# Kernel tuning notes

Hardware: AMD Instinct MI355X
Metric: run time of the kernel (lower is better)

## Reference

```python
import jax, jax.numpy as jnp
import numpy as np

B, L, D = 4096, 50, 64
NU, NI, NR = 100000, 100000, 5


def setup_inputs() -> dict:
    key = jax.random.key(0)
    ks = jax.random.split(key, 16)
    s = 0.02
    inp = {
        "nodes_v": jax.random.randint(ks[0], (B,), 0, NI),
        "neigh_u": jax.random.randint(ks[1], (B, L), 0, NU),
        "neigh_r": jax.random.randint(ks[2], (B, L), 0, NR),
        "embed_u": jax.random.normal(ks[3], (NU, D)) * s,
        "embed_i": jax.random.normal(ks[4], (NI, D)) * s,
        "embed_r": jax.random.normal(ks[5], (NR, D)) * s,
        # gv MLP: Linear(2D,D) ReLU Linear(D,D) ReLU Linear(D,D)
        "gv_w1": jax.random.normal(ks[6], (2 * D, D)) * s, "gv_b1": jnp.zeros((D,)),
        "gv_w2": jax.random.normal(ks[7], (D, D)) * s,     "gv_b2": jnp.zeros((D,)),
        "gv_w3": jax.random.normal(ks[8], (D, D)) * s,     "gv_b3": jnp.zeros((D,)),
        # attention MLP: Linear(2D,D) ReLU Linear(D,D) ReLU Linear(D,1), softmax over neighbors
        "att_w1": jax.random.normal(ks[9], (2 * D, D)) * s, "att_b1": jnp.zeros((D,)),
        "att_w2": jax.random.normal(ks[10], (D, D)) * s,    "att_b2": jnp.zeros((D,)),
        "att_w3": jax.random.normal(ks[11], (D, 1)) * s,    "att_b3": jnp.zeros((1,)),
        # combine: Linear(2D,D) ReLU Linear(D,D) ReLU
        "wr1_w": jax.random.normal(ks[12], (2 * D, D)) * s, "wr1_b": jnp.zeros((D,)),
        "wr2_w": jax.random.normal(ks[13], (D, D)) * s,     "wr2_b": jnp.zeros((D,)),
    }
    return inp


def reference(nodes_v, neigh_u, neigh_r, embed_u, embed_i, embed_r,
              gv_w1, gv_b1, gv_w2, gv_b2, gv_w3, gv_b3,
              att_w1, att_b1, att_w2, att_b2, att_w3, att_b3,
              wr1_w, wr1_b, wr2_w, wr2_b):
    qj = embed_i[nodes_v]            # [B, D] item reps
    pt = embed_u[neigh_u]            # [B, L, D] neighbor user reps
    er = embed_r[neigh_r]            # [B, L, D] rating reps
    # fusion MLP g(.)
    x = jnp.concatenate([pt, er], axis=-1)                    # [B, L, 2D]
    h = jax.nn.relu(x @ gv_w1 + gv_b1)
    h = jax.nn.relu(h @ gv_w2 + gv_b2)
    fjt = h @ gv_w3 + gv_b3                                   # [B, L, D]
    # attention over neighbors (dropout is identity in eval mode)
    q_rep = jnp.broadcast_to(qj[:, None, :], fjt.shape)       # [B, L, D]
    a = jnp.concatenate([fjt, q_rep], axis=-1)                # [B, L, 2D]
    a = jax.nn.relu(a @ att_w1 + att_b1)
    a = jax.nn.relu(a @ att_w2 + att_b2)
    scores = (a @ att_w3 + att_b3)[..., 0]                    # [B, L]
    mu = jax.nn.softmax(scores, axis=1)                       # softmax over neighbors
    zj = jnp.einsum("bld,bl->bd", fjt, mu)                   # weighted aggregation
    # combine aggregated neighborhood with item's own embedding (2D -> D)
    z = jax.nn.relu(jnp.concatenate([zj, qj], axis=-1) @ wr1_w + wr1_b)
    out = jax.nn.relu(z @ wr2_w + wr2_b)                      # [B, D]
    return out
```

## Files before the change

kernel.cpp:

```cpp
#include <hip/hip_runtime.h>

typedef __bf16 bf16;
typedef short s16x8 __attribute__((ext_vector_type(8)));
typedef __bf16 b16x8 __attribute__((ext_vector_type(8)));
typedef float f32x4 __attribute__((ext_vector_type(4)));

#define B_   4096
#define L_   50
#define SH   72

#define OFF_W1F  0
#define OFF_W2F  8192
#define OFF_W3F  12288
#define OFF_WCF  16384
#define OFF_A2F  20480
#define OFF_R1T  24576
#define OFF_R2T  32768
#define WT_TOTAL 36864
#define BIAS1P_BYTE 73728
#define CQ_BYTE     73984
#define EU16_BYTE   1122560
#define ER16_BYTE   13922560
#define WS_NEED     13923200

#define PREP_W_BLOCKS 145
#define CQ_BLOCKS     32
#define CONV_THREADS  800040
#define CONV_BLOCKS   3126

__device__ __forceinline__ unsigned short f2b(float f) {
    __bf16 h = (__bf16)f;
    return __builtin_bit_cast(unsigned short, h);
}
__device__ __forceinline__ unsigned pack2(float a, float b) {
    return (unsigned)f2b(a) | ((unsigned)f2b(b) << 16);
}
__device__ __forceinline__ s16x8 mkfrag(float4 a, float4 b) {
    union { s16x8 v; unsigned u[4]; } r;
    r.u[0] = pack2(a.x, a.y); r.u[1] = pack2(a.z, a.w);
    r.u[2] = pack2(b.x, b.y); r.u[3] = pack2(b.z, b.w);
    return r.v;
}
__device__ __forceinline__ f32x4 mfma16(s16x8 a, s16x8 b, f32x4 c) {
    return __builtin_amdgcn_mfma_f32_16x16x32_bf16(a, b, c, 0, 0, 0);
}

extern "C" __global__ void prep_all(const float* __restrict__ w1, const float* __restrict__ w2,
                                    const float* __restrict__ w3, const float* __restrict__ a1,
                                    const float* __restrict__ a2, const float* __restrict__ r1,
                                    const float* __restrict__ r2, const float* __restrict__ gb3,
                                    const float* __restrict__ ab1,
                                    const int* __restrict__ nodes_v, const float* __restrict__ embed_i,
                                    const float* __restrict__ embed_u, const float* __restrict__ embed_r,
                                    bf16* __restrict__ wt, float* __restrict__ bias1p,
                                    float* __restrict__ cq,
                                    bf16* __restrict__ eu16, bf16* __restrict__ er16)
{
    if (blockIdx.x >= PREP_W_BLOCKS + CQ_BLOCKS) {
        long t = (long)(blockIdx.x - PREP_W_BLOCKS - CQ_BLOCKS) * 256 + threadIdx.x;
        if (t < 800000) {
            const float* s = embed_u + t * 8;
            float4 a = *(const float4*)s, b = *(const float4*)(s + 4);
            *(s16x8*)(eu16 + t * 8) = mkfrag(a, b);
        } else if (t < CONV_THREADS) {
            long r = (t - 800000) * 8;
            const float* s = embed_r + r;
            float4 a = *(const float4*)s, b = *(const float4*)(s + 4);
            *(s16x8*)(er16 + r) = mkfrag(a, b);
        }
        return;
    }
    if (blockIdx.x >= PREP_W_BLOCKS) {
        int wv   = (blockIdx.x - PREP_W_BLOCKS) * 4 + (threadIdx.x >> 6);
        int lane = threadIdx.x & 63, m = lane & 15, quad = lane >> 4;
        int base = wv * 32;
        int i0 = base + m, i1 = base + 16 + m;
        int v0 = nodes_v[i0], v1 = nodes_v[i1];

        s16x8 bfr[8];
#pragma unroll
        for (int kt = 0; kt < 2; ++kt)
#pragma unroll
            for (int nt = 0; nt < 4; ++nt) {
                const float* src = a1 + (64 + kt * 32 + quad * 8) * 64 + nt * 16 + m;
                union { s16x8 v; unsigned u[4]; } fr;
#pragma unroll
                for (int jj = 0; jj < 4; ++jj)
                    fr.u[jj] = pack2(src[(2 * jj) * 64], src[(2 * jj + 1) * 64]);
                bfr[kt * 4 + nt] = fr.v;
            }

        f32x4 ac0[4] = {}, ac1[4] = {};
#pragma unroll
        for (int kt = 0; kt < 2; ++kt) {
            const float* q0 = embed_i + (size_t)v0 * 64 + kt * 32 + quad * 8;
            const float* q1 = embed_i + (size_t)v1 * 64 + kt * 32 + quad * 8;
            s16x8 aq0 = mkfrag(*(const float4*)q0, *(const float4*)(q0 + 4));
            s16x8 aq1 = mkfrag(*(const float4*)q1, *(const float4*)(q1 + 4));
#pragma unroll
            for (int nt = 0; nt < 4; ++nt) {
                ac0[nt] = mfma16(aq0, bfr[kt * 4 + nt], ac0[nt]);
                ac1[nt] = mfma16(aq1, bfr[kt * 4 + nt], ac1[nt]);
            }
        }
#pragma unroll
        for (int nt = 0; nt < 4; ++nt) {
            int c = nt * 16 + m;
#pragma unroll
            for (int r4 = 0; r4 < 4; ++r4) {
                cq[(base + quad * 4 + r4) * 64 + c]      = ac0[nt][r4];
                cq[(base + 16 + quad * 4 + r4) * 64 + c] = ac1[nt][r4];
            }
        }
        return;
    }
    int i = blockIdx.x * 256 + threadIdx.x;
    if (i >= WT_TOTAL + 64) return;
    if (i >= WT_TOTAL) {
        int n = i - WT_TOTAL;
        float s0 = ab1[n], s1 = 0.f, s2 = 0.f, s3 = 0.f;
#pragma unroll
        for (int t = 0; t < 64; t += 4) {
            s0 = fmaf(gb3[t],     a1[t * 64 + n],       s0);
            s1 = fmaf(gb3[t + 1], a1[(t + 1) * 64 + n], s1);
            s2 = fmaf(gb3[t + 2], a1[(t + 2) * 64 + n], s2);
            s3 = fmaf(gb3[t + 3], a1[(t + 3) * 64 + n], s3);
        }
        bias1p[n] = (s0 + s1) + (s2 + s3);
        return;
    }
    float val;
    if (i < OFF_R1T) {
        int off, kind;
        if      (i < OFF_W2F) { off = OFF_W1F; kind = 0; }
        else if (i < OFF_W3F) { off = OFF_W2F; kind = 1; }
        else if (i < OFF_WCF) { off = OFF_W3F; kind = 2; }
        else if (i < OFF_A2F) { off = OFF_WCF; kind = 3; }
        else                  { off = OFF_A2F; kind = 4; }
        int local = i - off;
        int f = local >> 9, lane = (local >> 3) & 63, j = local & 7;
        int kt = f >> 2, nt = f & 3, quad = lane >> 4, m = lane & 15;
        int k = kt * 32 + quad * 8 + j;
        int n = nt * 16 + m;
        if (kind == 0)      val = w1[k * 64 + n];
        else if (kind == 1) val = w2[k * 64 + n];
        else if (kind == 2) val = w3[k * 64 + n];
        else if (kind == 4) val = a2[k * 64 + n];
        else {
            float s0 = 0.f, s1 = 0.f, s2 = 0.f, s3 = 0.f;
#pragma unroll
            for (int t = 0; t < 64; t += 4) {
                float4 w = *(const float4*)(w3 + k * 64 + t);
                s0 = fmaf(w.x, a1[t * 64 + n],       s0);
                s1 = fmaf(w.y, a1[(t + 1) * 64 + n], s1);
                s2 = fmaf(w.z, a1[(t + 2) * 64 + n], s2);
                s3 = fmaf(w.w, a1[(t + 3) * 64 + n], s3);
            }
            val = (s0 + s1) + (s2 + s3);
        }
    }
    else if (i < OFF_R2T) { int li = i - OFF_R1T; int n = li >> 7, k = li & 127; val = r1[k * 64 + n]; }
    else                  { int li = i - OFF_R2T; int n = li >> 6, k = li & 63;  val = r2[k * 64 + n]; }
    wt[i] = (bf16)val;
}

template<bool BF16E>
__global__ void __launch_bounds__(256, 2)
dense_fused(const int* __restrict__ nodes_v, const int* __restrict__ neigh_u,
            const int* __restrict__ neigh_r,
            const float* __restrict__ embed_u, const float* __restrict__ embed_i,
            const float* __restrict__ embed_r,
            const float* __restrict__ gv_b1, const float* __restrict__ gv_b2,
            const float* __restrict__ gv_b3,
            const float* __restrict__ att_b2, const float* __restrict__ att_w3,
            const float* __restrict__ wr1_b, const float* __restrict__ wr2_b,
            const bf16* __restrict__ wt, const bf16* __restrict__ eu16,
            const bf16* __restrict__ er16, const float* __restrict__ cq,
            const float* __restrict__ bias1p, float* __restrict__ out)
{
    __shared__ __align__(16) bf16 H[128 * SH];
    __shared__ float zp[4 * 64];
    __shared__ float swm[4 * 2];
    __shared__ float qsh[2 * 64];

    const int tid = threadIdx.x;
    const int lane = tid & 63, wave = tid >> 6;
    const int m = lane & 15, quad = lane >> 4;
    const int b0 = blockIdx.x * 2;
    const int rw0 = wave * 32;
    const int item_w = rw0 >> 6;
    const int lbase = rw0 & 63;

    const int bw = b0 + item_w;
    const int l0 = min(lbase + m, L_ - 1);
    const int l1 = min(lbase + 16 + m, L_ - 1);
    const int u0 = neigh_u[bw * L_ + l0], u1 = neigh_u[bw * L_ + l1];
    const int v0 = neigh_r[bw * L_ + l0], v1 = neigh_r[bw * L_ + l1];

    float cs4[4];
#pragma unroll
    for (int nt = 0; nt < 4; ++nt) {
        int c = nt * 16 + m;
        cs4[nt] = cq[bw * 64 + c] + bias1p[c];
    }

    bf16* Hw = H + rw0 * SH;
    bf16* H0 = Hw;
    bf16* H1 = Hw + 16 * SH;

    {
        f32x4 ac0[4] = {}, ac1[4] = {};
        if constexpr (BF16E) {
            const bf16* p00 = eu16 + (size_t)u0 * 64;
            const bf16* p01 = eu16 + (size_t)u1 * 64;
            const bf16* p10 = er16 + v0 * 64;
            const bf16* p11 = er16 + v1 * 64;
#pragma unroll
            for (int kt = 0; kt < 4; ++kt) {
                const bf16* s0p = (kt < 2 ? p00 : p10) + (kt & 1) * 32 + quad * 8;
                const bf16* s1p = (kt < 2 ? p01 : p11) + (kt & 1) * 32 + quad * 8;
                s16x8 a0 = *(const s16x8*)s0p;
                s16x8 a1 = *(const s16x8*)s1p;
#pragma unroll
                for (int nt = 0; nt < 4; ++nt) {
                    s16x8 bfr = *(const s16x8*)(wt + OFF_W1F + (kt * 4 + nt) * 512 + lane * 8);
                    ac0[nt] = mfma16(a0, bfr, ac0[nt]);
                    ac1[nt] = mfma16(a1, bfr, ac1[nt]);
                }
            }
        } else {
            const float* b00 = embed_u + (size_t)u0 * 64;
            const float* b01 = embed_u + (size_t)u1 * 64;
            const float* b10 = embed_r + v0 * 64;
            const float* b11 = embed_r + v1 * 64;
#pragma unroll
            for (int kt = 0; kt < 4; ++kt) {
                const float* s0p = (kt < 2 ? b00 : b10) + (kt & 1) * 32 + quad * 8;
                const float* s1p = (kt < 2 ? b01 : b11) + (kt & 1) * 32 + quad * 8;
                float4 a0a = *(const float4*)s0p, a0b = *(const float4*)(s0p + 4);
                float4 a1a = *(const float4*)s1p, a1b = *(const float4*)(s1p + 4);
                s16x8 a0 = mkfrag(a0a, a0b);
                s16x8 a1 = mkfrag(a1a, a1b);
#pragma unroll
                for (int nt = 0; nt < 4; ++nt) {
                    s16x8 bfr = *(const s16x8*)(wt + OFF_W1F + (kt * 4 + nt) * 512 + lane * 8);
                    ac0[nt] = mfma16(a0, bfr, ac0[nt]);
                    ac1[nt] = mfma16(a1, bfr, ac1[nt]);
                }
            }
        }
#pragma unroll
        for (int nt = 0; nt < 4; ++nt) {
            int c = nt * 16 + m;
            float bv = gv_b1[c];
#pragma unroll
            for (int r4 = 0; r4 < 4; ++r4) {
                H0[(quad * 4 + r4) * SH + c] = (bf16)fmaxf(ac0[nt][r4] + bv, 0.f);
                H1[(quad * 4 + r4) * SH + c] = (bf16)fmaxf(ac1[nt][r4] + bv, 0.f);
            }
        }
    }

    {
        f32x4 ac0[4] = {}, ac1[4] = {};
#pragma unroll
        for (int kt = 0; kt < 2; ++kt) {
            s16x8 a0 = *(const s16x8*)(H0 + m * SH + kt * 32 + quad * 8);
            s16x8 a1 = *(const s16x8*)(H1 + m * SH + kt * 32 + quad * 8);
#pragma unroll
            for (int nt = 0; nt < 4; ++nt) {
                s16x8 bfr = *(const s16x8*)(wt + OFF_W2F + (kt * 4 + nt) * 512 + lane * 8);
                ac0[nt] = mfma16(a0, bfr, ac0[nt]);
                ac1[nt] = mfma16(a1, bfr, ac1[nt]);
            }
        }
#pragma unroll
        for (int nt = 0; nt < 4; ++nt) {
            int c = nt * 16 + m;
            float bv = gv_b2[c];
#pragma unroll
            for (int r4 = 0; r4 < 4; ++r4) {
                H0[(quad * 4 + r4) * SH + c] = (bf16)fmaxf(ac0[nt][r4] + bv, 0.f);
                H1[(quad * 4 + r4) * SH + c] = (bf16)fmaxf(ac1[nt][r4] + bv, 0.f);
            }
        }
    }

    f32x4 aF0[4] = {}, aF1[4] = {};
    {
        f32x4 aA0[4] = {}, aA1[4] = {};
#pragma unroll
        for (int kt = 0; kt < 2; ++kt) {
            s16x8 a0 = *(const s16x8*)(H0 + m * SH + kt * 32 + quad * 8);
            s16x8 a1 = *(const s16x8*)(H1 + m * SH + kt * 32 + quad * 8);
#pragma unroll
            for (int nt = 0; nt < 4; ++nt) {
                s16x8 bF = *(const s16x8*)(wt + OFF_W3F + (kt * 4 + nt) * 512 + lane * 8);
                s16x8 bA = *(const s16x8*)(wt + OFF_WCF + (kt * 4 + nt) * 512 + lane * 8);
                aF0[nt] = mfma16(a0, bF, aF0[nt]);
                aF1[nt] = mfma16(a1, bF, aF1[nt]);
                aA0[nt] = mfma16(a0, bA, aA0[nt]);
                aA1[nt] = mfma16(a1, bA, aA1[nt]);
            }
        }
#pragma unroll
        for (int nt = 0; nt < 4; ++nt) {
            int c = nt * 16 + m;
#pragma unroll
            for (int r4 = 0; r4 < 4; ++r4) {
                H0[(quad * 4 + r4) * SH + c] = (bf16)fmaxf(aA0[nt][r4] + cs4[nt], 0.f);
                H1[(quad * 4 + r4) * SH + c] = (bf16)fmaxf(aA1[nt][r4] + cs4[nt], 0.f);
            }
        }
    }

    float s0[4], s1[4];
    {
        f32x4 ac0[4] = {}, ac1[4] = {};
#pragma unroll
        for (int kt = 0; kt < 2; ++kt) {
            s16x8 a0 = *(const s16x8*)(H0 + m * SH + kt * 32 + quad * 8);
            s16x8 a1 = *(const s16x8*)(H1 + m * SH + kt * 32 + quad * 8);
#pragma unroll
            for (int nt = 0; nt < 4; ++nt) {
                s16x8 bfr = *(const s16x8*)(wt + OFF_A2F + (kt * 4 + nt) * 512 + lane * 8);
                ac0[nt] = mfma16(a0, bfr, ac0[nt]);
                ac1[nt] = mfma16(a1, bfr, ac1[nt]);
            }
        }
#pragma unroll
        for (int r4 = 0; r4 < 4; ++r4) { s0[r4] = 0.f; s1[r4] = 0.f; }
#pragma unroll
        for (int nt = 0; nt < 4; ++nt) {
            int c = nt * 16 + m;
            float b2v = att_b2[c], w3v = att_w3[c];
#pragma unroll
            for (int r4 = 0; r4 < 4; ++r4) {
                s0[r4] += fmaxf(ac0[nt][r4] + b2v, 0.f) * w3v;
                s1[r4] += fmaxf(ac1[nt][r4] + b2v, 0.f) * w3v;
            }
        }
#pragma unroll
        for (int mask = 1; mask < 16; mask <<= 1)
#pragma unroll
            for (int r4 = 0; r4 < 4; ++r4) {
                s0[r4] += __shfl_xor(s0[r4], mask);
                s1[r4] += __shfl_xor(s1[r4], mask);
            }
    }

    {
        const int r0b = lbase + quad * 4;
        float mloc = -1e30f;
#pragma unroll
        for (int r4 = 0; r4 < 4; ++r4) {
            if (r0b + r4 < L_)      mloc = fmaxf(mloc, s0[r4]);
            if (r0b + 16 + r4 < L_) mloc = fmaxf(mloc, s1[r4]);
        }
        mloc = fmaxf(mloc, __shfl_xor(mloc, 16));
        mloc = fmaxf(mloc, __shfl_xor(mloc, 32));

        float e0[4], e1[4], ssum = 0.f;
#pragma unroll
        for (int r4 = 0; r4 < 4; ++r4) {
            e0[r4] = (r0b + r4 < L_)      ? __expf(s0[r4] - mloc) : 0.f;
            e1[r4] = (r0b + 16 + r4 < L_) ? __expf(s1[r4] - mloc) : 0.f;
            ssum += e0[r4] + e1[r4];
        }
        ssum += __shfl_xor(ssum, 16);
        ssum += __shfl_xor(ssum, 32);

        float z[4] = {0.f, 0.f, 0.f, 0.f};
#pragma unroll
        for (int r4 = 0; r4 < 4; ++r4)
#pragma unroll
            for (int nt = 0; nt < 4; ++nt)
                z[nt] += aF0[nt][r4] * e0[r4] + aF1[nt][r4] * e1[r4];
#pragma unroll
        for (int nt = 0; nt < 4; ++nt) {
            z[nt] += __shfl_xor(z[nt], 16);
            z[nt] += __shfl_xor(z[nt], 32);
        }
        if (quad == 0) {
#pragma unroll
            for (int nt = 0; nt < 4; ++nt) zp[wave * 64 + nt * 16 + m] = z[nt];
        }
        if (lane == 0) { swm[wave * 2] = ssum; swm[wave * 2 + 1] = mloc; }
    }
    __syncthreads();

    if ((wave & 1) == 0) {
        const int item = wave >> 1;
        const int d = lane;
        float ma = swm[wave * 2 + 1],      mb = swm[(wave + 1) * 2 + 1];
        float sa = swm[wave * 2],          sb = swm[(wave + 1) * 2];
        float M  = fmaxf(ma, mb);
        float fa = __expf(ma - M), fb = __expf(mb - M);
        float zj = (fa * zp[wave * 64 + d] + fb * zp[(wave + 1) * 64 + d])
                 / (fa * sa + fb * sb) + gv_b3[d];

        float* zsh = zp + wave * 64;
        zsh[d] = zj;
        qsh[item * 64 + d] = embed_i[nodes_v[b0 + item] * 64 + d];

        float accz = wr1_b[d];
        const bf16* r1 = wt + OFF_R1T + d * 128;
#pragma unroll
        for (int k8 = 0; k8 < 8; ++k8) {
            b16x8 wv = *(const b16x8*)(r1 + k8 * 8);
#pragma unroll
            for (int j = 0; j < 8; ++j) accz = fmaf((float)wv[j], zsh[k8 * 8 + j], accz);
        }
#pragma unroll
        for (int k8 = 0; k8 < 8; ++k8) {
            b16x8 wv = *(const b16x8*)(r1 + 64 + k8 * 8);
#pragma unroll
            for (int j = 0; j < 8; ++j) accz = fmaf((float)wv[j], qsh[item * 64 + k8 * 8 + j], accz);
        }
        zsh[d] = fmaxf(accz, 0.f);

        float acco = wr2_b[d];
        const bf16* r2 = wt + OFF_R2T + d * 64;
#pragma unroll
        for (int k8 = 0; k8 < 8; ++k8) {
            b16x8 wv = *(const b16x8*)(r2 + k8 * 8);
#pragma unroll
            for (int j = 0; j < 8; ++j) acco = fmaf((float)wv[j], zsh[k8 * 8 + j], acco);
        }
        out[(b0 + item) * 64 + d] = fmaxf(acco, 0.f);
    }
}

extern "C" void kernel_launch(void* const* d_in, const int* in_sizes, int n_in,
                              void* d_out, int out_size, void* d_ws, size_t ws_size,
                              hipStream_t stream)
{
    const int* nodes_v = (const int*)d_in[0];
    const int* neigh_u = (const int*)d_in[1];
    const int* neigh_r = (const int*)d_in[2];
    const float* embed_u = (const float*)d_in[3];
    const float* embed_i = (const float*)d_in[4];
    const float* embed_r = (const float*)d_in[5];
    const float* gv_w1  = (const float*)d_in[6];  const float* gv_b1 = (const float*)d_in[7];
    const float* gv_w2  = (const float*)d_in[8];  const float* gv_b2 = (const float*)d_in[9];
    const float* gv_w3  = (const float*)d_in[10]; const float* gv_b3 = (const float*)d_in[11];
    const float* att_w1 = (const float*)d_in[12]; const float* att_b1 = (const float*)d_in[13];
    const float* att_w2 = (const float*)d_in[14]; const float* att_b2 = (const float*)d_in[15];
    const float* att_w3 = (const float*)d_in[16]; const float* att_b3 = (const float*)d_in[17];
    const float* wr1_w  = (const float*)d_in[18]; const float* wr1_b = (const float*)d_in[19];
    const float* wr2_w  = (const float*)d_in[20]; const float* wr2_b = (const float*)d_in[21];
    (void)att_b3;

    bf16*  wt     = (bf16*)d_ws;
    float* bias1p = (float*)((char*)d_ws + BIAS1P_BYTE);
    float* cq     = (float*)((char*)d_ws + CQ_BYTE);
    bf16*  eu16   = (bf16*)((char*)d_ws + EU16_BYTE);
    bf16*  er16   = (bf16*)((char*)d_ws + ER16_BYTE);

    const bool big = ws_size >= (size_t)WS_NEED;
    const int prep_grid = PREP_W_BLOCKS + CQ_BLOCKS + (big ? CONV_BLOCKS : 0);

    prep_all<<<prep_grid, 256, 0, stream>>>(
        gv_w1, gv_w2, gv_w3, att_w1, att_w2, wr1_w, wr2_w, gv_b3, att_b1,
        nodes_v, embed_i, embed_u, embed_r, wt, bias1p, cq, eu16, er16);

    if (big) {
        dense_fused<true><<<B_ / 2, 256, 0, stream>>>(nodes_v, neigh_u, neigh_r,
                                                      embed_u, embed_i, embed_r,
                                                      gv_b1, gv_b2, gv_b3, att_b2, att_w3,
                                                      wr1_b, wr2_b, wt, eu16, er16,
                                                      cq, bias1p, (float*)d_out);
    } else {
        dense_fused<false><<<B_ / 2, 256, 0, stream>>>(nodes_v, neigh_u, neigh_r,
                                                       embed_u, embed_i, embed_r,
                                                       gv_b1, gv_b2, gv_b3, att_b2, att_w3,
                                                       wr1_b, wr2_b, wt, eu16, er16,
                                                       cq, bias1p, (float*)d_out);
    }
}
```

Baseline: 159.3 us.

## Process one batch item per single-wave block to drop cross-wave softmax merge

Restructures the fused kernel so that each 64-thread block (one wave) handles all 64 padded neighbor rows of a single item, instead of four waves sharing two items. This removes the shared-memory partial-softmax merge and the __syncthreads, lets each wave reuse every weight fragment across four row tiles, and uses nontemporal loads for the gathered embedding rows. In exchange each wave holds many more accumulators, which raises register pressure, and the final combine MLP now runs on every block rather than half the waves.

After: 177.4 us. 11.3% more time.

```diff
diff --git a/kernel.cpp b/kernel.cpp
--- a/kernel.cpp
+++ b/kernel.cpp
@@ -43,6 +43,9 @@
 }
 __device__ __forceinline__ f32x4 mfma16(s16x8 a, s16x8 b, f32x4 c) {
     return __builtin_amdgcn_mfma_f32_16x16x32_bf16(a, b, c, 0, 0, 0);
+}
+__device__ __forceinline__ s16x8 ntload16(const bf16* p) {
+    return __builtin_nontemporal_load((const s16x8*)p);
 }
 
 extern "C" __global__ void prep_all(const float* __restrict__ w1, const float* __restrict__ w2,
@@ -165,7 +168,7 @@
 }
 
 template<bool BF16E>
-__global__ void __launch_bounds__(256, 2)
+__global__ void __launch_bounds__(64, 3)
 dense_fused(const int* __restrict__ nodes_v, const int* __restrict__ neigh_u,
             const int* __restrict__ neigh_r,
             const float* __restrict__ embed_u, const float* __restrict__ embed_i,
@@ -178,256 +181,250 @@
             const bf16* __restrict__ er16, const float* __restrict__ cq,
             const float* __restrict__ bias1p, float* __restrict__ out)
 {
-    __shared__ __align__(16) bf16 H[128 * SH];
-    __shared__ float zp[4 * 64];
-    __shared__ float swm[4 * 2];
-    __shared__ float qsh[2 * 64];
-
-    const int tid = threadIdx.x;
-    const int lane = tid & 63, wave = tid >> 6;
+    __shared__ __align__(16) bf16 H[64 * SH];
+
+    const int lane = threadIdx.x;
     const int m = lane & 15, quad = lane >> 4;
-    const int b0 = blockIdx.x * 2;
-    const int rw0 = wave * 32;
-    const int item_w = rw0 >> 6;
-    const int lbase = rw0 & 63;
-
-    const int bw = b0 + item_w;
-    const int l0 = min(lbase + m, L_ - 1);
-    const int l1 = min(lbase + 16 + m, L_ - 1);
-    const int u0 = neigh_u[bw * L_ + l0], u1 = neigh_u[bw * L_ + l1];
-    const int v0 = neigh_r[bw * L_ + l0], v1 = neigh_r[bw * L_ + l1];
+    const int b = blockIdx.x;
+
+    int un[4], vn[4];
+#pragma unroll
+    for (int t = 0; t < 4; ++t) {
+        int l = min(t * 16 + m, L_ - 1);
+        un[t] = neigh_u[b * L_ + l];
+        vn[t] = neigh_r[b * L_ + l];
+    }
 
     float cs4[4];
 #pragma unroll
     for (int nt = 0; nt < 4; ++nt) {
         int c = nt * 16 + m;
-        cs4[nt] = cq[bw * 64 + c] + bias1p[c];
-    }
-
-    bf16* Hw = H + rw0 * SH;
-    bf16* H0 = Hw;
-    bf16* H1 = Hw + 16 * SH;
-
-    {
-        f32x4 ac0[4] = {}, ac1[4] = {};
-        if constexpr (BF16E) {
-            const bf16* p00 = eu16 + (size_t)u0 * 64;
-            const bf16* p01 = eu16 + (size_t)u1 * 64;
-            const bf16* p10 = er16 + v0 * 64;
-            const bf16* p11 = er16 + v1 * 64;
-#pragma unroll
-            for (int kt = 0; kt < 4; ++kt) {
-                const bf16* s0p = (kt < 2 ? p00 : p10) + (kt & 1) * 32 + quad * 8;
-                const bf16* s1p = (kt < 2 ? p01 : p11) + (kt & 1) * 32 + quad * 8;
-                s16x8 a0 = *(const s16x8*)s0p;
-                s16x8 a1 = *(const s16x8*)s1p;
+        cs4[nt] = cq[b * 64 + c] + bias1p[c];
+    }
+
+    {
+        f32x4 ac[4][4] = {};
+#pragma unroll
+        for (int kt = 0; kt < 4; ++kt) {
+            s16x8 bfr[4];
+#pragma unroll
+            for (int nt = 0; nt < 4; ++nt)
+                bfr[nt] = *(const s16x8*)(wt + OFF_W1F + (kt * 4 + nt) * 512 + lane * 8);
+#pragma unroll
+            for (int t = 0; t < 4; ++t) {
+                s16x8 a;
+                if constexpr (BF16E) {
+                    const bf16* src = (kt < 2 ? eu16 + (size_t)un[t] * 64
+                                              : er16 + (size_t)vn[t] * 64)
+                                      + (kt & 1) * 32 + quad * 8;
+                    a = ntload16(src);
+                } else {
+                    const float* src = (kt < 2 ? embed_u + (size_t)un[t] * 64
+                                               : embed_r + (size_t)vn[t] * 64)
+                                       + (kt & 1) * 32 + quad * 8;
+                    a = mkfrag(*(const float4*)src, *(const float4*)(src + 4));
+                }
+#pragma unroll
+                for (int nt = 0; nt < 4; ++nt)
+                    ac[t][nt] = mfma16(a, bfr[nt], ac[t][nt]);
+            }
+        }
+#pragma unroll
+        for (int nt = 0; nt < 4; ++nt) {
+            int c = nt * 16 + m;
+            float bv = gv_b1[c];
+#pragma unroll
+            for (int t = 0; t < 4; ++t)
+#pragma unroll
+                for (int r4 = 0; r4 < 4; ++r4)
+                    H[(t * 16 + quad * 4 + r4) * SH + c] = (bf16)fmaxf(ac[t][nt][r4] + bv, 0.f);
+        }
+    }
+
+    {
+        f32x4 ac[4][4] = {};
+#pragma unroll
+        for (int kt = 0; kt < 2; ++kt) {
+            s16x8 bfr[4];
+#pragma unroll
+            for (int nt = 0; nt < 4; ++nt)
+                bfr[nt] = *(const s16x8*)(wt + OFF_W2F + (kt * 4 + nt) * 512 + lane * 8);
+#pragma unroll
+            for (int t = 0; t < 4; ++t) {
+                s16x8 a = *(const s16x8*)(H + (t * 16 + m) * SH + kt * 32 + quad * 8);
+#pragma unroll
+                for (int nt = 0; nt < 4; ++nt)
+                    ac[t][nt] = mfma16(a, bfr[nt], ac[t][nt]);
+            }
+        }
+#pragma unroll
+        for (int nt = 0; nt < 4; ++nt) {
+            int c = nt * 16 + m;
+            float bv = gv_b2[c];
+#pragma unroll
+            for (int t = 0; t < 4; ++t)
+#pragma unroll
+                for (int r4 = 0; r4 < 4; ++r4)
+                    H[(t * 16 + quad * 4 + r4) * SH + c] = (bf16)fmaxf(ac[t][nt][r4] + bv, 0.f);
+        }
+    }
+
+    f32x4 aF[4][4] = {};
+    {
+        f32x4 aA[4][4] = {};
+#pragma unroll
+        for (int kt = 0; kt < 2; ++kt) {
+            s16x8 bF[4], bA[4];
+#pragma unroll
+            for (int nt = 0; nt < 4; ++nt) {
+                bF[nt] = *(const s16x8*)(wt + OFF_W3F + (kt * 4 + nt) * 512 + lane * 8);
+                bA[nt] = *(const s16x8*)(wt + OFF_WCF + (kt * 4 + nt) * 512 + lane * 8);
+            }
+#pragma unroll
+            for (int t = 0; t < 4; ++t) {
+                s16x8 a = *(const s16x8*)(H + (t * 16 + m) * SH + kt * 32 + quad * 8);
 #pragma unroll
                 for (int nt = 0; nt < 4; ++nt) {
-                    s16x8 bfr = *(const s16x8*)(wt + OFF_W1F + (kt * 4 + nt) * 512 + lane * 8);
-                    ac0[nt] = mfma16(a0, bfr, ac0[nt]);
-                    ac1[nt] = mfma16(a1, bfr, ac1[nt]);
+                    aF[t][nt] = mfma16(a, bF[nt], aF[t][nt]);
+                    aA[t][nt] = mfma16(a, bA[nt], aA[t][nt]);
                 }
             }
-        } else {
-            const float* b00 = embed_u + (size_t)u0 * 64;
-            const float* b01 = embed_u + (size_t)u1 * 64;
-            const float* b10 = embed_r + v0 * 64;
-            const float* b11 = embed_r + v1 * 64;
-#pragma unroll
-            for (int kt = 0; kt < 4; ++kt) {
-                const float* s0p = (kt < 2 ? b00 : b10) + (kt & 1) * 32 + quad * 8;
-                const float* s1p = (kt < 2 ? b01 : b11) + (kt & 1) * 32 + quad * 8;
-                float4 a0a = *(const float4*)s0p, a0b = *(const float4*)(s0p + 4);
-                float4 a1a = *(const float4*)s1p, a1b = *(const float4*)(s1p + 4);
-                s16x8 a0 = mkfrag(a0a, a0b);
-                s16x8 a1 = mkfrag(a1a, a1b);
-#pragma unroll
-                for (int nt = 0; nt < 4; ++nt) {
-                    s16x8 bfr = *(const s16x8*)(wt + OFF_W1F + (kt * 4 + nt) * 512 + lane * 8);
-                    ac0[nt] = mfma16(a0, bfr, ac0[nt]);
-                    ac1[nt] = mfma16(a1, bfr, ac1[nt]);
-                }
-            }
-        }
-#pragma unroll
-        for (int nt = 0; nt < 4; ++nt) {
-            int c = nt * 16 + m;
-            float bv = gv_b1[c];
-#pragma unroll
-            for (int r4 = 0; r4 < 4; ++r4) {
-                H0[(quad * 4 + r4) * SH + c] = (bf16)fmaxf(ac0[nt][r4] + bv, 0.f);
-                H1[(quad * 4 + r4) * SH + c] = (bf16)fmaxf(ac1[nt][r4] + bv, 0.f);
-            }
-        }
-    }
-
-    {
-        f32x4 ac0[4] = {}, ac1[4] = {};
+        }
+#pragma unroll
+        for (int nt = 0; nt < 4; ++nt) {
+            int c = nt * 16 + m;
+#pragma unroll
+            for (int t = 0; t < 4; ++t)
+#pragma unroll
+                for (int r4 = 0; r4 < 4; ++r4)
+                    H[(t * 16 + quad * 4 + r4) * SH + c] = (bf16)fmaxf(aA[t][nt][r4] + cs4[nt], 0.f);
+        }
+    }
+
+    float sc[4][4];
+    {
+        f32x4 ac[4][4] = {};
 #pragma unroll
         for (int kt = 0; kt < 2; ++kt) {
-            s16x8 a0 = *(const s16x8*)(H0 + m * SH + kt * 32 + quad * 8);
-            s16x8 a1 = *(const s16x8*)(H1 + m * SH + kt * 32 + quad * 8);
-#pragma unroll
-            for (int nt = 0; nt < 4; ++nt) {
-                s16x8 bfr = *(const s16x8*)(wt + OFF_W2F + (kt * 4 + nt) * 512 + lane * 8);
-                ac0[nt] = mfma16(a0, bfr, ac0[nt]);
-                ac1[nt] = mfma16(a1, bfr, ac1[nt]);
-            }
-        }
-#pragma unroll
-        for (int nt = 0; nt < 4; ++nt) {
-            int c = nt * 16 + m;
-            float bv = gv_b2[c];
-#pragma unroll
-            for (int r4 = 0; r4 < 4; ++r4) {
-                H0[(quad * 4 + r4) * SH + c] = (bf16)fmaxf(ac0[nt][r4] + bv, 0.f);
-                H1[(quad * 4 + r4) * SH + c] = (bf16)fmaxf(ac1[nt][r4] + bv, 0.f);
-            }
-        }
-    }
-
-    f32x4 aF0[4] = {}, aF1[4] = {};
-    {
-        f32x4 aA0[4] = {}, aA1[4] = {};
-#pragma unroll
-        for (int kt = 0; kt < 2; ++kt) {
-            s16x8 a0 = *(const s16x8*)(H0 + m * SH + kt * 32 + quad * 8);
-            s16x8 a1 = *(const s16x8*)(H1 + m * SH + kt * 32 + quad * 8);
-#pragma unroll
-            for (int nt = 0; nt < 4; ++nt) {
-                s16x8 bF = *(const s16x8*)(wt + OFF_W3F + (kt * 4 + nt) * 512 + lane * 8);
-                s16x8 bA = *(const s16x8*)(wt + OFF_WCF + (kt * 4 + nt) * 512 + lane * 8);
-                aF0[nt] = mfma16(a0, bF, aF0[nt]);
-                aF1[nt] = mfma16(a1, bF, aF1[nt]);
-                aA0[nt] = mfma16(a0, bA, aA0[nt]);
-                aA1[nt] = mfma16(a1, bA, aA1[nt]);
-            }
-        }
-#pragma unroll
-        for (int nt = 0; nt < 4; ++nt) {
-            int c = nt * 16 + m;
-#pragma unroll
-            for (int r4 = 0; r4 < 4; ++r4) {
-                H0[(quad * 4 + r4) * SH + c] = (bf16)fmaxf(aA0[nt][r4] + cs4[nt], 0.f);
-                H1[(quad * 4 + r4) * SH + c] = (bf16)fmaxf(aA1[nt][r4] + cs4[nt], 0.f);
-            }
-        }
-    }
-
-    float s0[4], s1[4];
-    {
-        f32x4 ac0[4] = {}, ac1[4] = {};
-#pragma unroll
-        for (int kt = 0; kt < 2; ++kt) {
-            s16x8 a0 = *(const s16x8*)(H0 + m * SH + kt * 32 + quad * 8);
-            s16x8 a1 = *(const s16x8*)(H1 + m * SH + kt * 32 + quad * 8);
-#pragma unroll
-            for (int nt = 0; nt < 4; ++nt) {
-                s16x8 bfr = *(const s16x8*)(wt + OFF_A2F + (kt * 4 + nt) * 512 + lane * 8);
-                ac0[nt] = mfma16(a0, bfr, ac0[nt]);
-                ac1[nt] = mfma16(a1, bfr, ac1[nt]);
-            }
-        }
-#pragma unroll
-        for (int r4 = 0; r4 < 4; ++r4) { s0[r4] = 0.f; s1[r4] = 0.f; }
+            s16x8 bfr[4];
+#pragma unroll
+            for (int nt = 0; nt < 4; ++nt)
+                bfr[nt] = *(const s16x8*)(wt + OFF_A2F + (kt * 4 + nt) * 512 + lane * 8);
+#pragma unroll
+            for (int t = 0; t < 4; ++t) {
+                s16x8 a = *(const s16x8*)(H + (t * 16 + m) * SH + kt * 32 + quad * 8);
+#pragma unroll
+                for (int nt = 0; nt < 4; ++nt)
+                    ac[t][nt] = mfma16(a, bfr[nt], ac[t][nt]);
+            }
+        }
+#pragma unroll
+        for (int t = 0; t < 4; ++t)
+#pragma unroll
+            for (int r4 = 0; r4 < 4; ++r4) sc[t][r4] = 0.f;
 #pragma unroll
         for (int nt = 0; nt < 4; ++nt) {
             int c = nt * 16 + m;
             float b2v = att_b2[c], w3v = att_w3[c];
 #pragma unroll
-            for (int r4 = 0; r4 < 4; ++r4) {
-                s0[r4] += fmaxf(ac0[nt][r4] + b2v, 0.f) * w3v;
-                s1[r4] += fmaxf(ac1[nt][r4] + b2v, 0.f) * w3v;
-            }
+            for (int t = 0; t < 4; ++t)
+#pragma unroll
+                for (int r4 = 0; r4 < 4; ++r4)
+                    sc[t][r4] += fmaxf(ac[t][nt][r4] + b2v, 0.f) * w3v;
         }
 #pragma unroll
         for (int mask = 1; mask < 16; mask <<= 1)
 #pragma unroll
-            for (int r4 = 0; r4 < 4; ++r4) {
-                s0[r4] += __shfl_xor(s0[r4], mask);
-                s1[r4] += __shfl_xor(s1[r4], mask);
-            }
-    }
-
-    {
-        const int r0b = lbase + quad * 4;
+            for (int t = 0; t < 4; ++t)
+#pragma unroll
+                for (int r4 = 0; r4 < 4; ++r4)
+                    sc[t][r4] += __shfl_xor(sc[t][r4], mask);
+    }
+
+    float z[4], ssum;
+    {
         float mloc = -1e30f;
 #pragma unroll
-        for (int r4 = 0; r4 < 4; ++r4) {
-            if (r0b + r4 < L_)      mloc = fmaxf(mloc, s0[r4]);
-            if (r0b + 16 + r4 < L_) mloc = fmaxf(mloc, s1[r4]);
-        }
+        for (int t = 0; t < 4; ++t)
+#pragma unroll
+            for (int r4 = 0; r4 < 4; ++r4)
+                if (t * 16 + quad * 4 + r4 < L_) mloc = fmaxf(mloc, sc[t][r4]);
         mloc = fmaxf(mloc, __shfl_xor(mloc, 16));
         mloc = fmaxf(mloc, __shfl_xor(mloc, 32));
 
-        float e0[4], e1[4], ssum = 0.f;
-#pragma unroll
-        for (int r4 = 0; r4 < 4; ++r4) {
-            e0[r4] = (r0b + r4 < L_)      ? __expf(s0[r4] - mloc) : 0.f;
-            e1[r4] = (r0b + 16 + r4 < L_) ? __expf(s1[r4] - mloc) : 0.f;
-            ssum += e0[r4] + e1[r4];
-        }
+        float e[4][4];
+        ssum = 0.f;
+#pragma unroll
+        for (int t = 0; t < 4; ++t)
+#pragma unroll
+            for (int r4 = 0; r4 < 4; ++r4) {
+                e[t][r4] = (t * 16 + quad * 4 + r4 < L_) ? __expf(sc[t][r4] - mloc) : 0.f;
+                ssum += e[t][r4];
+            }
         ssum += __shfl_xor(ssum, 16);
         ssum += __shfl_xor(ssum, 32);
 
-        float z[4] = {0.f, 0.f, 0.f, 0.f};
-#pragma unroll
-        for (int r4 = 0; r4 < 4; ++r4)
-#pragma unroll
-            for (int nt = 0; nt < 4; ++nt)
-                z[nt] += aF0[nt][r4] * e0[r4] + aF1[nt][r4] * e1[r4];
+#pragma unroll
+        for (int nt = 0; nt < 4; ++nt) z[nt] = 0.f;
+#pragma unroll
+        for (int t = 0; t < 4; ++t)
+#pragma unroll
+            for (int r4 = 0; r4 < 4; ++r4)
+#pragma unroll
+                for (int nt = 0; nt < 4; ++nt)
+                    z[nt] += aF[t][nt][r4] * e[t][r4];
 #pragma unroll
         for (int nt = 0; nt < 4; ++nt) {
             z[nt] += __shfl_xor(z[nt], 16);
             z[nt] += __shfl_xor(z[nt], 32);
         }
-        if (quad == 0) {
-#pragma unroll
-            for (int nt = 0; nt < 4; ++nt) zp[wave * 64 + nt * 16 + m] = z[nt];
-        }
-        if (lane == 0) { swm[wave * 2] = ssum; swm[wave * 2 + 1] = mloc; }
-    }
-    __syncthreads();
-
-    if ((wave & 1) == 0) {
-        const int item = wave >> 1;
+    }
+
+    {
+        float* zsh = (float*)H;
+        float* qsh = zsh + 64;
+#pragma unroll
+        for (int nt = 0; nt < 4; ++nt) {
+            int c = nt * 16 + m;
+            zsh[c] = z[nt] / ssum + gv_b3[c];
+        }
         const int d = lane;
-        float ma = swm[wave * 2 + 1],      mb = swm[(wave + 1) * 2 + 1];
-        float sa = swm[wave * 2],          sb = swm[(wave + 1) * 2];
-        float M  = fmaxf(ma, mb);
-        float fa = __expf(ma - M), fb = __expf(mb - M);
-        float zj = (fa * zp[wave * 64 + d] + fb * zp[(wave + 1) * 64 + d])
-                 / (fa * sa + fb * sb) + gv_b3[d];
-
-        float* zsh = zp + wave * 64;
-        zsh[d] = zj;
-        qsh[item * 64 + d] = embed_i[nodes_v[b0 + item] * 64 + d];
-
-        float accz = wr1_b[d];
+        qsh[d] = embed_i[(size_t)nodes_v[b] * 64 + d];
+
+        float p0 = wr1_b[d], p1 = 0.f;
         const bf16* r1 = wt + OFF_R1T + d * 128;
 #pragma unroll
         for (int k8 = 0; k8 < 8; ++k8) {
             b16x8 wv = *(const b16x8*)(r1 + k8 * 8);
 #pragma unroll
-            for (int j = 0; j < 8; ++j) accz = fmaf((float)wv[j], zsh[k8 * 8 + j], accz);
+            for (int j = 0; j < 8; j += 2) {
+                p0 = fmaf((float)wv[j],     zsh[k8 * 8 + j],     p0);
+                p1 = fmaf((float)wv[j + 1], zsh[k8 * 8 + j + 1], p1);
+            }
         }
 #pragma unroll
         for (int k8 = 0; k8 < 8; ++k8) {
             b16x8 wv = *(const b16x8*)(r1 + 64 + k8 * 8);
 #pragma unroll
-            for (int j = 0; j < 8; ++j) accz = fmaf((float)wv[j], qsh[item * 64 + k8 * 8 + j], accz);
-        }
-        zsh[d] = fmaxf(accz, 0.f);
-
-        float acco = wr2_b[d];
+            for (int j = 0; j < 8; j += 2) {
+                p0 = fmaf((float)wv[j],     qsh[k8 * 8 + j],     p0);
+                p1 = fmaf((float)wv[j + 1], qsh[k8 * 8 + j + 1], p1);
+            }
+        }
+        zsh[d] = fmaxf(p0 + p1, 0.f);
+
+        float q0 = wr2_b[d], q1 = 0.f;
         const bf16* r2 = wt + OFF_R2T + d * 64;
 #pragma unroll
         for (int k8 = 0; k8 < 8; ++k8) {
             b16x8 wv = *(const b16x8*)(r2 + k8 * 8);
 #pragma unroll
-            for (int j = 0; j < 8; ++j) acco = fmaf((float)wv[j], zsh[k8 * 8 + j], acco);
-        }
-        out[(b0 + item) * 64 + d] = fmaxf(acco, 0.f);
+            for (int j = 0; j < 8; j += 2) {
+                q0 = fmaf((float)wv[j],     zsh[k8 * 8 + j],     q0);
+                q1 = fmaf((float)wv[j + 1], zsh[k8 * 8 + j + 1], q1);
+            }
+        }
+        out[(size_t)b * 64 + d] = fmaxf(q0 + q1, 0.f);
     }
 }
 
@@ -465,16 +462,16 @@
         nodes_v, embed_i, embed_u, embed_r, wt, bias1p, cq, eu16, er16);
 
     if (big) {
-        dense_fused<true><<<B_ / 2, 256, 0, stream>>>(nodes_v, neigh_u, neigh_r,
-                                                      embed_u, embed_i, embed_r,
-                                                      gv_b1, gv_b2, gv_b3, att_b2, att_w3,
-                                                      wr1_b, wr2_b, wt, eu16, er16,
-                                                      cq, bias1p, (float*)d_out);
+        dense_fused<true><<<B_, 64, 0, stream>>>(nodes_v, neigh_u, neigh_r,
+                                                 embed_u, embed_i, embed_r,
+                                                 gv_b1, gv_b2, gv_b3, att_b2, att_w3,
+                                                 wr1_b, wr2_b, wt, eu16, er16,
+                                                 cq, bias1p, (float*)d_out);
     } else {
-        dense_fused<false><<<B_ / 2, 256, 0, stream>>>(nodes_v, neigh_u, neigh_r,
-                                                       embed_u, embed_i, embed_r,
-                                                       gv_b1, gv_b2, gv_b3, att_b2, att_w3,
-                                                       wr1_b, wr2_b, wt, eu16, er16,
-                                                       cq, bias1p, (float*)d_out);
-    }
-}
+        dense_fused<false><<<B_, 64, 0, stream>>>(nodes_v, neigh_u, neigh_r,
+                                                  embed_u, embed_i, embed_r,
+                                                  gv_b1, gv_b2, gv_b3, att_b2, att_w3,
+                                                  wr1_b, wr2_b, wt, eu16, er16,
+                                                  cq, bias1p, (float*)d_out);
+    }
+}
```

## Precompute first fusion layer per user and rating table row

Applied to the files above, without the earlier changes.

Computes the first gv layer (user half via MFMA, rating half plus bias in scalar) for every row of the user and rating tables in the prep kernel, storing fp32 results in workspace. The main kernel then gathers these partial sums, adds them, applies ReLU and writes bf16 to shared memory, skipping the first-layer MFMAs. This replaces the per-call bf16 table conversion, but doubles the bytes written by prep and the bytes per gathered row, since the results are stored in fp32.

Result: slower. 168.5 us (+5.8%).

```diff
diff --git a/kernel.cpp b/kernel.cpp
--- a/kernel.cpp
+++ b/kernel.cpp
@@ -17,20 +17,23 @@
 #define OFF_R1T  24576
 #define OFF_R2T  32768
 #define WT_TOTAL 36864
+#define HERR_N   320
 #define BIAS1P_BYTE 73728
 #define CQ_BYTE     73984
-#define EU16_BYTE   1122560
-#define ER16_BYTE   13922560
-#define WS_NEED     13923200
-
-#define PREP_W_BLOCKS 145
+#define HERR_BYTE   1122560
+#define H1U_BYTE    1123840
+#define WS_NEED     26723840
+
+#define PREP_W_BLOCKS 146
 #define CQ_BLOCKS     32
-#define CONV_THREADS  800040
-#define CONV_BLOCKS   3126
+#define H1U_BLOCKS    782
 
 __device__ __forceinline__ unsigned short f2b(float f) {
     __bf16 h = (__bf16)f;
     return __builtin_bit_cast(unsigned short, h);
+}
+__device__ __forceinline__ float bround(float f) {
+    return (float)(__bf16)f;
 }
 __device__ __forceinline__ unsigned pack2(float a, float b) {
     return (unsigned)f2b(a) | ((unsigned)f2b(b) << 16);
@@ -49,24 +52,54 @@
                                     const float* __restrict__ w3, const float* __restrict__ a1,
                                     const float* __restrict__ a2, const float* __restrict__ r1,
                                     const float* __restrict__ r2, const float* __restrict__ gb3,
-                                    const float* __restrict__ ab1,
+                                    const float* __restrict__ ab1, const float* __restrict__ gb1,
                                     const int* __restrict__ nodes_v, const float* __restrict__ embed_i,
                                     const float* __restrict__ embed_u, const float* __restrict__ embed_r,
                                     bf16* __restrict__ wt, float* __restrict__ bias1p,
-                                    float* __restrict__ cq,
-                                    bf16* __restrict__ eu16, bf16* __restrict__ er16)
+                                    float* __restrict__ cq, float* __restrict__ herr,
+                                    float* __restrict__ h1u)
 {
     if (blockIdx.x >= PREP_W_BLOCKS + CQ_BLOCKS) {
-        long t = (long)(blockIdx.x - PREP_W_BLOCKS - CQ_BLOCKS) * 256 + threadIdx.x;
-        if (t < 800000) {
-            const float* s = embed_u + t * 8;
-            float4 a = *(const float4*)s, b = *(const float4*)(s + 4);
-            *(s16x8*)(eu16 + t * 8) = mkfrag(a, b);
-        } else if (t < CONV_THREADS) {
-            long r = (t - 800000) * 8;
-            const float* s = embed_r + r;
-            float4 a = *(const float4*)s, b = *(const float4*)(s + 4);
-            *(s16x8*)(er16 + r) = mkfrag(a, b);
+        int wv   = (blockIdx.x - PREP_W_BLOCKS - CQ_BLOCKS) * 4 + (threadIdx.x >> 6);
+        int base = wv * 32;
+        if (base >= 100000) return;
+        int lane = threadIdx.x & 63, m = lane & 15, quad = lane >> 4;
+        int i0 = base + m, i1 = base + 16 + m;
+
+        s16x8 bfr[8];
+#pragma unroll
+        for (int kt = 0; kt < 2; ++kt)
+#pragma unroll
+            for (int nt = 0; nt < 4; ++nt) {
+                const float* src = w1 + (kt * 32 + quad * 8) * 64 + nt * 16 + m;
+                union { s16x8 v; unsigned u[4]; } fr;
+#pragma unroll
+                for (int jj = 0; jj < 4; ++jj)
+                    fr.u[jj] = pack2(src[(2 * jj) * 64], src[(2 * jj + 1) * 64]);
+                bfr[kt * 4 + nt] = fr.v;
+            }
+
+        f32x4 ac0[4] = {}, ac1[4] = {};
+#pragma unroll
+        for (int kt = 0; kt < 2; ++kt) {
+            const float* q0 = embed_u + (size_t)i0 * 64 + kt * 32 + quad * 8;
+            const float* q1 = embed_u + (size_t)i1 * 64 + kt * 32 + quad * 8;
+            s16x8 aq0 = mkfrag(*(const float4*)q0, *(const float4*)(q0 + 4));
+            s16x8 aq1 = mkfrag(*(const float4*)q1, *(const float4*)(q1 + 4));
+#pragma unroll
+            for (int nt = 0; nt < 4; ++nt) {
+                ac0[nt] = mfma16(aq0, bfr[kt * 4 + nt], ac0[nt]);
+                ac1[nt] = mfma16(aq1, bfr[kt * 4 + nt], ac1[nt]);
+            }
+        }
+#pragma unroll
+        for (int nt = 0; nt < 4; ++nt) {
+            int c = nt * 16 + m;
+#pragma unroll
+            for (int r4 = 0; r4 < 4; ++r4) {
+                h1u[(size_t)(base + quad * 4 + r4) * 64 + c]      = ac0[nt][r4];
+                h1u[(size_t)(base + 16 + quad * 4 + r4) * 64 + c] = ac1[nt][r4];
+            }
         }
         return;
     }
@@ -115,7 +148,22 @@
         return;
     }
     int i = blockIdx.x * 256 + threadIdx.x;
-    if (i >= WT_TOTAL + 64) return;
+    if (i >= WT_TOTAL + 64 + HERR_N) return;
+    if (i >= WT_TOTAL + 64) {
+        int i2 = i - (WT_TOTAL + 64);
+        int r = i2 >> 6, n = i2 & 63;
+        float s0 = gb1[n], s1 = 0.f, s2 = 0.f, s3 = 0.f;
+        const float* er = embed_r + r * 64;
+#pragma unroll
+        for (int k = 0; k < 64; k += 4) {
+            s0 = fmaf(bround(er[k]),     bround(w1[(64 + k) * 64 + n]),     s0);
+            s1 = fmaf(bround(er[k + 1]), bround(w1[(64 + k + 1) * 64 + n]), s1);
+            s2 = fmaf(bround(er[k + 2]), bround(w1[(64 + k + 2) * 64 + n]), s2);
+            s3 = fmaf(bround(er[k + 3]), bround(w1[(64 + k + 3) * 64 + n]), s3);
+        }
+        herr[i2] = (s0 + s1) + (s2 + s3);
+        return;
+    }
     if (i >= WT_TOTAL) {
         int n = i - WT_TOTAL;
         float s0 = ab1[n], s1 = 0.f, s2 = 0.f, s3 = 0.f;
@@ -164,7 +212,7 @@
     wt[i] = (bf16)val;
 }
 
-template<bool BF16E>
+template<bool PRE>
 __global__ void __launch_bounds__(256, 2)
 dense_fused(const int* __restrict__ nodes_v, const int* __restrict__ neigh_u,
             const int* __restrict__ neigh_r,
@@ -174,8 +222,8 @@
             const float* __restrict__ gv_b3,
             const float* __restrict__ att_b2, const float* __restrict__ att_w3,
             const float* __restrict__ wr1_b, const float* __restrict__ wr2_b,
-            const bf16* __restrict__ wt, const bf16* __restrict__ eu16,
-            const bf16* __restrict__ er16, const float* __restrict__ cq,
+            const bf16* __restrict__ wt, const float* __restrict__ h1u,
+            const float* __restrict__ herr, const float* __restrict__ cq,
             const float* __restrict__ bias1p, float* __restrict__ out)
 {
     __shared__ __align__(16) bf16 H[128 * SH];
@@ -208,45 +256,49 @@
     bf16* H0 = Hw;
     bf16* H1 = Hw + 16 * SH;
 
-    {
+    if constexpr (PRE) {
+        const float* hu0 = h1u + (size_t)u0 * 64;
+        const float* hu1 = h1u + (size_t)u1 * 64;
+        const float* he0 = herr + v0 * 64;
+        const float* he1 = herr + v1 * 64;
+#pragma unroll
+        for (int half = 0; half < 2; ++half) {
+            const int cb = half * 32 + quad * 8;
+            float4 x0 = *(const float4*)(hu0 + cb), x1 = *(const float4*)(hu0 + cb + 4);
+            float4 y0 = *(const float4*)(he0 + cb), y1 = *(const float4*)(he0 + cb + 4);
+            union { s16x8 v; unsigned u[4]; } ra;
+            ra.u[0] = pack2(fmaxf(x0.x + y0.x, 0.f), fmaxf(x0.y + y0.y, 0.f));
+            ra.u[1] = pack2(fmaxf(x0.z + y0.z, 0.f), fmaxf(x0.w + y0.w, 0.f));
+            ra.u[2] = pack2(fmaxf(x1.x + y1.x, 0.f), fmaxf(x1.y + y1.y, 0.f));
+            ra.u[3] = pack2(fmaxf(x1.z + y1.z, 0.f), fmaxf(x1.w + y1.w, 0.f));
+            *(s16x8*)(H0 + m * SH + cb) = ra.v;
+
+            float4 p0 = *(const float4*)(hu1 + cb), p1 = *(const float4*)(hu1 + cb + 4);
+            float4 q0 = *(const float4*)(he1 + cb), q1 = *(const float4*)(he1 + cb + 4);
+            union { s16x8 v; unsigned u[4]; } rb;
+            rb.u[0] = pack2(fmaxf(p0.x + q0.x, 0.f), fmaxf(p0.y + q0.y, 0.f));
+            rb.u[1] = pack2(fmaxf(p0.z + q0.z, 0.f), fmaxf(p0.w + q0.w, 0.f));
+            rb.u[2] = pack2(fmaxf(p1.x + q1.x, 0.f), fmaxf(p1.y + q1.y, 0.f));
+            rb.u[3] = pack2(fmaxf(p1.z + q1.z, 0.f), fmaxf(p1.w + q1.w, 0.f));
+            *(s16x8*)(H1 + m * SH + cb) = rb.v;
+        }
+    } else {
         f32x4 ac0[4] = {}, ac1[4] = {};
-        if constexpr (BF16E) {
-            const bf16* p00 = eu16 + (size_t)u0 * 64;
-            const bf16* p01 = eu16 + (size_t)u1 * 64;
-            const bf16* p10 = er16 + v0 * 64;
-            const bf16* p11 = er16 + v1 * 64;
-#pragma unroll
-            for (int kt = 0; kt < 4; ++kt) {
-                const bf16* s0p = (kt < 2 ? p00 : p10) + (kt & 1) * 32 + quad * 8;
-                const bf16* s1p = (kt < 2 ? p01 : p11) + (kt & 1) * 32 + quad * 8;
-                s16x8 a0 = *(const s16x8*)s0p;
-                s16x8 a1 = *(const s16x8*)s1p;
-#pragma unroll
-                for (int nt = 0; nt < 4; ++nt) {
-                    s16x8 bfr = *(const s16x8*)(wt + OFF_W1F + (kt * 4 + nt) * 512 + lane * 8);
-                    ac0[nt] = mfma16(a0, bfr, ac0[nt]);
-                    ac1[nt] = mfma16(a1, bfr, ac1[nt]);
-                }
-            }
-        } else {
-            const float* b00 = embed_u + (size_t)u0 * 64;
-            const float* b01 = embed_u + (size_t)u1 * 64;
-            const float* b10 = embed_r + v0 * 64;
-            const float* b11 = embed_r + v1 * 64;
-#pragma unroll
-            for (int kt = 0; kt < 4; ++kt) {
-                const float* s0p = (kt < 2 ? b00 : b10) + (kt & 1) * 32 + quad * 8;
-                const float* s1p = (kt < 2 ? b01 : b11) + (kt & 1) * 32 + quad * 8;
-                float4 a0a = *(const float4*)s0p, a0b = *(const float4*)(s0p + 4);
-                float4 a1a = *(const float4*)s1p, a1b = *(const float4*)(s1p + 4);
-                s16x8 a0 = mkfrag(a0a, a0b);
-                s16x8 a1 = mkfrag(a1a, a1b);
-#pragma unroll
-                for (int nt = 0; nt < 4; ++nt) {
-                    s16x8 bfr = *(const s16x8*)(wt + OFF_W1F + (kt * 4 + nt) * 512 + lane * 8);
-                    ac0[nt] = mfma16(a0, bfr, ac0[nt]);
-                    ac1[nt] = mfma16(a1, bfr, ac1[nt]);
-                }
+        const float* b00 = embed_u + (size_t)u0 * 64;
+        const float* b01 = embed_u + (size_t)u1 * 64;
+        const float* b10 = embed_r + v0 * 64;
+        const float* b11 = embed_r + v1 * 64;
+#pragma unroll
+        for (int kt = 0; kt < 4; ++kt) {
+            const float* s0p = (kt < 2 ? b00 : b10) + (kt & 1) * 32 + quad * 8;
+            const float* s1p = (kt < 2 ? b01 : b11) + (kt & 1) * 32 + quad * 8;
+            s16x8 a0 = mkfrag(*(const float4*)s0p, *(const float4*)(s0p + 4));
+            s16x8 a1 = mkfrag(*(const float4*)s1p, *(const float4*)(s1p + 4));
+#pragma unroll
+            for (int nt = 0; nt < 4; ++nt) {
+                s16x8 bfr = *(const s16x8*)(wt + OFF_W1F + (kt * 4 + nt) * 512 + lane * 8);
+                ac0[nt] = mfma16(a0, bfr, ac0[nt]);
+                ac1[nt] = mfma16(a1, bfr, ac1[nt]);
             }
         }
 #pragma unroll
@@ -454,27 +506,27 @@
     bf16*  wt     = (bf16*)d_ws;
     float* bias1p = (float*)((char*)d_ws + BIAS1P_BYTE);
     float* cq     = (float*)((char*)d_ws + CQ_BYTE);
-    bf16*  eu16   = (bf16*)((char*)d_ws + EU16_BYTE);
-    bf16*  er16   = (bf16*)((char*)d_ws + ER16_BYTE);
+    float* herr   = (float*)((char*)d_ws + HERR_BYTE);
+    float* h1u    = (float*)((char*)d_ws + H1U_BYTE);
 
     const bool big = ws_size >= (size_t)WS_NEED;
-    const int prep_grid = PREP_W_BLOCKS + CQ_BLOCKS + (big ? CONV_BLOCKS : 0);
+    const int prep_grid = PREP_W_BLOCKS + CQ_BLOCKS + (big ? H1U_BLOCKS : 0);
 
     prep_all<<<prep_grid, 256, 0, stream>>>(
-        gv_w1, gv_w2, gv_w3, att_w1, att_w2, wr1_w, wr2_w, gv_b3, att_b1,
-        nodes_v, embed_i, embed_u, embed_r, wt, bias1p, cq, eu16, er16);
+        gv_w1, gv_w2, gv_w3, att_w1, att_w2, wr1_w, wr2_w, gv_b3, att_b1, gv_b1,
+        nodes_v, embed_i, embed_u, embed_r, wt, bias1p, cq, herr, h1u);
 
     if (big) {
         dense_fused<true><<<B_ / 2, 256, 0, stream>>>(nodes_v, neigh_u, neigh_r,
                                                       embed_u, embed_i, embed_r,
                                                       gv_b1, gv_b2, gv_b3, att_b2, att_w3,
-                                                      wr1_b, wr2_b, wt, eu16, er16,
+                                                      wr1_b, wr2_b, wt, h1u, herr,
                                                       cq, bias1p, (float*)d_out);
     } else {
         dense_fused<false><<<B_ / 2, 256, 0, stream>>>(nodes_v, neigh_u, neigh_r,
                                                        embed_u, embed_i, embed_r,
                                                        gv_b1, gv_b2, gv_b3, att_b2, att_w3,
-                                                       wr1_b, wr2_b, wt, eu16, er16,
+                                                       wr1_b, wr2_b, wt, h1u, herr,
                                                        cq, bias1p, (float*)d_out);
     }
 }
```
